# Optimization experiments

Measured on AMD Instinct MI355X. Metric: run time of the kernel, lower is better.

The kernel has to match this reference:

```python
import jax, jax.numpy as jnp
import numpy as np

N = 50000      # num_nodes
DEG = 16       # edges per node
E = N * DEG    # 800k edges
IN_DIM = 512
OUT_DIM = 128


def _glorot(key, shape):
    limit = np.sqrt(6.0 / (shape[0] + shape[1]))
    return jax.random.uniform(key, shape, jnp.float32, -limit, limit)


def setup_inputs() -> dict:
    key = jax.random.key(0)
    k1, k2, k3 = jax.random.split(key, 3)
    x = jax.random.normal(k1, (N, IN_DIM), jnp.float32)
    W = _glorot(k2, (IN_DIM, OUT_DIM))
    a = _glorot(k3, (OUT_DIM, 1))
    # structured, duplicate-free edge list: node i -> (i+1..i+DEG) mod N
    rows = np.repeat(np.arange(N, dtype=np.int32), DEG)
    offs = np.tile(np.arange(1, DEG + 1, dtype=np.int32), N)
    cols = (rows + offs) % N
    edge_index = jnp.asarray(np.stack([rows, cols]), jnp.int32)  # [2, E]
    return {"x": x, "W": W, "a": a, "edge_index": edge_index}


def reference(x, W, a, edge_index):
    # sparse mm (math-identical dense form); dropout_rate=0 -> identity
    h = x @ W                                    # [N, OUT]
    rows, cols = edge_index[0], edge_index[1]
    h_i = h[rows]                                # [E, OUT] gather
    h_j = h[cols]                                # [E, OUT] gather
    scores = jax.nn.relu(jnp.abs(h_i - h_j) @ a)[:, 0]  # [E]
    # sparse row-wise softmax (segment softmax over destination rows)
    m = jax.ops.segment_max(scores, rows, num_segments=N)   # [N]
    p = jnp.exp(scores - m[rows])                            # [E]
    s = jax.ops.segment_sum(p, rows, num_segments=N)         # [N]
    attn = p / s[rows]                                       # [E]
    return h, attn
```

## Files before the change

kernel.cpp:

```cpp
#include <hip/hip_runtime.h>
#include <hip/hip_bf16.h>

#define NNODES 50000
#define DEG 16
#define NEDGES (NNODES * DEG)
#define IND 512
#define OUTD 128

#define BM 64
#define CK 64
#define NCH 8
#define NB 64
#define SROWS 80

typedef __attribute__((ext_vector_type(8))) short bf16x8;
typedef __attribute__((ext_vector_type(4))) float f32x4;

static __device__ __forceinline__ unsigned short f2bf(float f) {
    unsigned u = __builtin_bit_cast(unsigned, f);
    u += 0x7fffu + ((u >> 16) & 1u);
    return (unsigned short)(u >> 16);
}

static __device__ __forceinline__ bf16x8 pack8(float4 a, float4 b) {
    union { unsigned u[4]; bf16x8 v; } r;
    r.u[0] = (unsigned)f2bf(a.x) | ((unsigned)f2bf(a.y) << 16);
    r.u[1] = (unsigned)f2bf(a.z) | ((unsigned)f2bf(a.w) << 16);
    r.u[2] = (unsigned)f2bf(b.x) | ((unsigned)f2bf(b.y) << 16);
    r.u[3] = (unsigned)f2bf(b.z) | ((unsigned)f2bf(b.w) << 16);
    return r.v;
}

__global__ __launch_bounds__(256) void wt_kernel(const float* __restrict__ W,
                                                 unsigned short* __restrict__ Wt) {
    int flat = blockIdx.x * 256 + threadIdx.x;
    int n  = flat >> 7;
    int k4 = flat & 127;
    int k0 = k4 * 4;
    unsigned short v0 = f2bf(W[(k0 + 0) * OUTD + n]);
    unsigned short v1 = f2bf(W[(k0 + 1) * OUTD + n]);
    unsigned short v2 = f2bf(W[(k0 + 2) * OUTD + n]);
    unsigned short v3 = f2bf(W[(k0 + 3) * OUTD + n]);
    uint2 o;
    o.x = (unsigned)v0 | ((unsigned)v1 << 16);
    o.y = (unsigned)v2 | ((unsigned)v3 << 16);
    *reinterpret_cast<uint2*>(&Wt[n * IND + k0]) = o;
}

__global__ __launch_bounds__(256, 2) void gemm_kernel(const float* __restrict__ x,
                                                      const unsigned short* __restrict__ Wt,
                                                      float* __restrict__ h) {
    __shared__ __align__(16) unsigned char lds_[65536];

    const int tid  = threadIdx.x;
    const int lane = tid & 63;
    const int wid  = tid >> 6;
    const int l15  = lane & 15;
    const int kg   = lane >> 4;
    const int base = blockIdx.x * BM;
    const int wr   = wid * 16;

    f32x4 acc[8];
#pragma unroll
    for (int nt = 0; nt < 8; ++nt) acc[nt] = (f32x4){0.f, 0.f, 0.f, 0.f};

    auto stage = [&](int buf, int ch) {
        const int k0 = ch * CK;
#pragma unroll
        for (int p = 0; p < 4; ++p) {
            int f   = p * 256 + tid;
            int row = f >> 4;
            int g   = (f & 15) ^ (row & 7);
            int gr  = base + row; if (gr > NNODES - 1) gr = NNODES - 1;
            const float* gp = &x[(size_t)gr * IND + k0 + g * 4];
            unsigned char* lp = &lds_[(size_t)buf * 16384 + (size_t)f * 16];
            __builtin_amdgcn_global_load_lds((const unsigned int*)gp, (unsigned int*)lp, 16, 0, 0);
        }
#pragma unroll
        for (int p = 0; p < 4; ++p) {
            int f   = p * 256 + tid;
            int col = f >> 3;
            int g   = (f & 7) ^ (col & 7);
            const unsigned short* gp = &Wt[(size_t)col * IND + k0 + g * 8];
            unsigned char* lp = &lds_[32768 + (size_t)buf * 16384 + (size_t)f * 16];
            __builtin_amdgcn_global_load_lds((const unsigned int*)gp, (unsigned int*)lp, 16, 0, 0);
        }
    };

    stage(0, 0);

    int buf = 0;
    for (int ch = 0; ch < NCH; ++ch) {
        if (ch < NCH - 1) {
            stage(buf ^ 1, ch + 1);
            asm volatile("s_waitcnt vmcnt(8)" ::: "memory");
        } else {
            asm volatile("s_waitcnt vmcnt(0)" ::: "memory");
        }
        __builtin_amdgcn_s_barrier();

#pragma unroll
        for (int ks = 0; ks < 2; ++ks) {
            int arow = wr + l15;
            const unsigned char* ab = &lds_[(size_t)buf * 16384 + (size_t)arow * 256];
            int g0 = (ks * 8 + kg * 2) ^ (arow & 7);
            int g1 = (ks * 8 + kg * 2 + 1) ^ (arow & 7);
            float4 a0 = *reinterpret_cast<const float4*>(ab + g0 * 16);
            float4 a1 = *reinterpret_cast<const float4*>(ab + g1 * 16);
            bf16x8 af = pack8(a0, a1);
#pragma unroll
            for (int nt = 0; nt < 8; ++nt) {
                int col = nt * 16 + l15;
                int gB  = (ks * 4 + kg) ^ (col & 7);
                bf16x8 bv = *reinterpret_cast<const bf16x8*>(
                    &lds_[32768 + (size_t)buf * 16384 + (size_t)col * 128 + gB * 16]);
                acc[nt] = __builtin_amdgcn_mfma_f32_16x16x32_bf16(af, bv, acc[nt], 0, 0, 0);
            }
        }
        __builtin_amdgcn_s_barrier();
        buf ^= 1;
    }

#pragma unroll
    for (int q = 0; q < 4; ++q) {
        int grow = base + wr + kg * 4 + q;
        if (grow < NNODES) {
#pragma unroll
            for (int nt = 0; nt < 8; ++nt)
                h[(size_t)grow * OUTD + nt * 16 + l15] = acc[nt][q];
        }
    }
}

__global__ __launch_bounds__(256) void edge_kernel(const float* __restrict__ h,
                                                   const float* __restrict__ a,
                                                   const int* __restrict__ eidx,
                                                   float* __restrict__ attn) {
    extern __shared__ __align__(16) unsigned char hl[];

    const int tid  = threadIdx.x;
    const int base = blockIdx.x * NB;
    const int lane = tid & 63;
    const int wid  = tid >> 6;
    const int j    = lane >> 2;
    const int g    = lane & 3;

    float4 a4[8];
#pragma unroll
    for (int c = 0; c < 8; ++c)
        a4[c] = *reinterpret_cast<const float4*>(&a[c * 16 + g * 4]);

    for (int p = 0; p < 10; ++p) {
        int f    = p * 256 + tid;
        int row  = f >> 5;
        int blkp = f & 31;
        int blk  = blkp ^ ((row & 7) << 2);
        int gr   = base + row;
        if (gr >= NNODES) gr -= NNODES;
        float4 v = *reinterpret_cast<const float4*>(&h[(size_t)gr * OUTD + blk * 4]);
        *reinterpret_cast<float4*>(&hl[f * 16]) = v;
    }
    __syncthreads();

    const int* cols = eidx + NEDGES;
    for (int n = 0; n < 16; ++n) {
        int i = base + wid * 16 + n;
        if (i >= NNODES) break;
        int e   = i * DEG + j;
        int col = cols[e];
        int cr  = col - base;
        if (cr < 0) cr += NNODES;
        int ri = i - base;
        float s = 0.f;
        if (cr < SROWS) {
#pragma unroll
            for (int c = 0; c < 8; ++c) {
                int blk = c * 4 + g;
                float4 hi = *reinterpret_cast<const float4*>(&hl[ri * 512 + ((blk ^ ((ri & 7) << 2)) * 16)]);
                float4 hj = *reinterpret_cast<const float4*>(&hl[cr * 512 + ((blk ^ ((cr & 7) << 2)) * 16)]);
                s = fmaf(fabsf(hi.x - hj.x), a4[c].x, s);
                s = fmaf(fabsf(hi.y - hj.y), a4[c].y, s);
                s = fmaf(fabsf(hi.z - hj.z), a4[c].z, s);
                s = fmaf(fabsf(hi.w - hj.w), a4[c].w, s);
            }
        } else {
#pragma unroll
            for (int c = 0; c < 8; ++c) {
                int blk = c * 4 + g;
                float4 hi = *reinterpret_cast<const float4*>(&hl[ri * 512 + ((blk ^ ((ri & 7) << 2)) * 16)]);
                float4 hj = *reinterpret_cast<const float4*>(&h[(size_t)col * OUTD + blk * 4]);
                s = fmaf(fabsf(hi.x - hj.x), a4[c].x, s);
                s = fmaf(fabsf(hi.y - hj.y), a4[c].y, s);
                s = fmaf(fabsf(hi.z - hj.z), a4[c].z, s);
                s = fmaf(fabsf(hi.w - hj.w), a4[c].w, s);
            }
        }
        s += __shfl_xor(s, 1);
        s += __shfl_xor(s, 2);
        s = fmaxf(s, 0.f);
        float m = s;
        m = fmaxf(m, __shfl_xor(m, 4));
        m = fmaxf(m, __shfl_xor(m, 8));
        m = fmaxf(m, __shfl_xor(m, 16));
        m = fmaxf(m, __shfl_xor(m, 32));
        float pv = __expf(s - m);
        float S = pv;
        S += __shfl_xor(S, 4);
        S += __shfl_xor(S, 8);
        S += __shfl_xor(S, 16);
        S += __shfl_xor(S, 32);
        if (g == 0) attn[e] = pv / S;
    }
}

extern "C" void kernel_launch(void* const* d_in, const int* in_sizes, int n_in,
                              void* d_out, int out_size, void* d_ws, size_t ws_size,
                              hipStream_t stream) {
    const float* x  = (const float*)d_in[0];
    const float* W  = (const float*)d_in[1];
    const float* a  = (const float*)d_in[2];
    const int* eidx = (const int*)d_in[3];
    float* h    = (float*)d_out;
    float* attn = h + (size_t)NNODES * OUTD;
    unsigned short* Wt = (unsigned short*)d_ws;

    hipLaunchKernelGGL(wt_kernel, dim3(64), dim3(256), 0, stream, W, Wt);
    hipLaunchKernelGGL(gemm_kernel, dim3((NNODES + BM - 1) / BM), dim3(256), 0, stream, x, Wt, h);
    hipLaunchKernelGGL(edge_kernel, dim3((NNODES + NB - 1) / NB), dim3(256), SROWS * 512, stream,
                       h, a, eidx, attn);
}
```

Measured before the change: 61.26 us.

## Stage x through registers as bf16 in LDS and split GEMM waves by column

The GEMM now loads x rows into registers one chunk ahead, converts them to bf16 once per block, and writes them to a swizzled LDS buffer, instead of copying fp32 x tiles into LDS and converting per wave. This halves the A-tile LDS footprint, which allows three blocks per CU instead of two. Waves now split the 128 output columns, so each wave does a 64x32 tile with 4x2 MFMAs, rather than each wave taking 16 rows and all columns. The B prefetch is issued after the barrier and one of the two per-chunk barriers is removed. This relies on a single barrier per chunk being enough to stop the next chunk's writes from overwriting buffers still being read, which is a race risk.

```diff
diff --git a/kernel.cpp b/kernel.cpp
--- a/kernel.cpp
+++ b/kernel.cpp
@@ -47,10 +47,10 @@
     *reinterpret_cast<uint2*>(&Wt[n * IND + k0]) = o;
 }
 
-__global__ __launch_bounds__(256, 2) void gemm_kernel(const float* __restrict__ x,
+__global__ __launch_bounds__(256, 3) void gemm_kernel(const float* __restrict__ x,
                                                       const unsigned short* __restrict__ Wt,
                                                       float* __restrict__ h) {
-    __shared__ __align__(16) unsigned char lds_[65536];
+    __shared__ __align__(16) unsigned char lds_[49152];
 
     const int tid  = threadIdx.x;
     const int lane = tid & 63;
@@ -58,76 +58,105 @@
     const int l15  = lane & 15;
     const int kg   = lane >> 4;
     const int base = blockIdx.x * BM;
-    const int wr   = wid * 16;
-
-    f32x4 acc[8];
-#pragma unroll
-    for (int nt = 0; nt < 8; ++nt) acc[nt] = (f32x4){0.f, 0.f, 0.f, 0.f};
-
-    auto stage = [&](int buf, int ch) {
-        const int k0 = ch * CK;
-#pragma unroll
-        for (int p = 0; p < 4; ++p) {
-            int f   = p * 256 + tid;
-            int row = f >> 4;
-            int g   = (f & 15) ^ (row & 7);
-            int gr  = base + row; if (gr > NNODES - 1) gr = NNODES - 1;
-            const float* gp = &x[(size_t)gr * IND + k0 + g * 4];
-            unsigned char* lp = &lds_[(size_t)buf * 16384 + (size_t)f * 16];
-            __builtin_amdgcn_global_load_lds((const unsigned int*)gp, (unsigned int*)lp, 16, 0, 0);
-        }
+    const int wc   = wid * 32;
+
+    const int ar  = tid >> 2;
+    const int ag0 = (tid & 3) * 2;
+    int agr = base + ar; if (agr > NNODES - 1) agr = NNODES - 1;
+    const float* axp = &x[(size_t)agr * IND + ag0 * 8];
+
+    f32x4 acc[4][2];
+#pragma unroll
+    for (int mt = 0; mt < 4; ++mt)
+#pragma unroll
+        for (int nt = 0; nt < 2; ++nt) acc[mt][nt] = (f32x4){0.f, 0.f, 0.f, 0.f};
+
+    float4 rA[2][4];
+
+    auto stageB = [&](int buf, int ch) {
 #pragma unroll
         for (int p = 0; p < 4; ++p) {
             int f   = p * 256 + tid;
             int col = f >> 3;
             int g   = (f & 7) ^ (col & 7);
-            const unsigned short* gp = &Wt[(size_t)col * IND + k0 + g * 8];
-            unsigned char* lp = &lds_[32768 + (size_t)buf * 16384 + (size_t)f * 16];
+            const unsigned short* gp = &Wt[(size_t)col * IND + ch * CK + g * 8];
+            unsigned char* lp = &lds_[16384 + (size_t)buf * 16384 + (size_t)f * 16];
             __builtin_amdgcn_global_load_lds((const unsigned int*)gp, (unsigned int*)lp, 16, 0, 0);
         }
     };
 
-    stage(0, 0);
-
-    int buf = 0;
+    {
+        const float* p = axp;
+        rA[0][0] = *reinterpret_cast<const float4*>(p);
+        rA[0][1] = *reinterpret_cast<const float4*>(p + 4);
+        rA[0][2] = *reinterpret_cast<const float4*>(p + 8);
+        rA[0][3] = *reinterpret_cast<const float4*>(p + 12);
+    }
+    stageB(0, 0);
+
+#pragma unroll
     for (int ch = 0; ch < NCH; ++ch) {
+        const int par = ch & 1;
         if (ch < NCH - 1) {
-            stage(buf ^ 1, ch + 1);
-            asm volatile("s_waitcnt vmcnt(8)" ::: "memory");
+            const float* p = axp + (ch + 1) * CK;
+            rA[par ^ 1][0] = *reinterpret_cast<const float4*>(p);
+            rA[par ^ 1][1] = *reinterpret_cast<const float4*>(p + 4);
+            rA[par ^ 1][2] = *reinterpret_cast<const float4*>(p + 8);
+            rA[par ^ 1][3] = *reinterpret_cast<const float4*>(p + 12);
+            asm volatile("s_waitcnt vmcnt(4)" ::: "memory");
         } else {
             asm volatile("s_waitcnt vmcnt(0)" ::: "memory");
         }
+
+        {
+            bf16x8 q0 = pack8(rA[par][0], rA[par][1]);
+            bf16x8 q1 = pack8(rA[par][2], rA[par][3]);
+            unsigned char* aw = &lds_[(size_t)par * 8192 + (size_t)ar * 128];
+            *reinterpret_cast<bf16x8*>(aw + ((ag0 ^ (ar & 7)) * 16))       = q0;
+            *reinterpret_cast<bf16x8*>(aw + (((ag0 + 1) ^ (ar & 7)) * 16)) = q1;
+        }
+        asm volatile("s_waitcnt lgkmcnt(0)" ::: "memory");
         __builtin_amdgcn_s_barrier();
-
+        asm volatile("" ::: "memory");
+        __builtin_amdgcn_sched_barrier(0);
+
+        if (ch < NCH - 1) stageB(par ^ 1, ch + 1);
+
+        const unsigned char* Ab = &lds_[(size_t)par * 8192];
+        const unsigned char* Bb = &lds_[16384 + (size_t)par * 16384];
 #pragma unroll
         for (int ks = 0; ks < 2; ++ks) {
-            int arow = wr + l15;
-            const unsigned char* ab = &lds_[(size_t)buf * 16384 + (size_t)arow * 256];
-            int g0 = (ks * 8 + kg * 2) ^ (arow & 7);
-            int g1 = (ks * 8 + kg * 2 + 1) ^ (arow & 7);
-            float4 a0 = *reinterpret_cast<const float4*>(ab + g0 * 16);
-            float4 a1 = *reinterpret_cast<const float4*>(ab + g1 * 16);
-            bf16x8 af = pack8(a0, a1);
-#pragma unroll
-            for (int nt = 0; nt < 8; ++nt) {
-                int col = nt * 16 + l15;
-                int gB  = (ks * 4 + kg) ^ (col & 7);
-                bf16x8 bv = *reinterpret_cast<const bf16x8*>(
-                    &lds_[32768 + (size_t)buf * 16384 + (size_t)col * 128 + gB * 16]);
-                acc[nt] = __builtin_amdgcn_mfma_f32_16x16x32_bf16(af, bv, acc[nt], 0, 0, 0);
-            }
-        }
-        __builtin_amdgcn_s_barrier();
-        buf ^= 1;
-    }
-
-#pragma unroll
-    for (int q = 0; q < 4; ++q) {
-        int grow = base + wr + kg * 4 + q;
-        if (grow < NNODES) {
-#pragma unroll
-            for (int nt = 0; nt < 8; ++nt)
-                h[(size_t)grow * OUTD + nt * 16 + l15] = acc[nt][q];
+            bf16x8 af[4], bfv[2];
+#pragma unroll
+            for (int mt = 0; mt < 4; ++mt) {
+                int row = mt * 16 + l15;
+                af[mt] = *reinterpret_cast<const bf16x8*>(
+                    Ab + row * 128 + (((ks * 4 + kg) ^ (row & 7)) * 16));
+            }
+#pragma unroll
+            for (int nt = 0; nt < 2; ++nt) {
+                int col = wc + nt * 16 + l15;
+                bfv[nt] = *reinterpret_cast<const bf16x8*>(
+                    Bb + col * 128 + (((ks * 4 + kg) ^ (col & 7)) * 16));
+            }
+#pragma unroll
+            for (int mt = 0; mt < 4; ++mt)
+#pragma unroll
+                for (int nt = 0; nt < 2; ++nt)
+                    acc[mt][nt] = __builtin_amdgcn_mfma_f32_16x16x32_bf16(af[mt], bfv[nt], acc[mt][nt], 0, 0, 0);
+        }
+    }
+
+#pragma unroll
+    for (int mt = 0; mt < 4; ++mt) {
+#pragma unroll
+        for (int q = 0; q < 4; ++q) {
+            int grow = base + mt * 16 + kg * 4 + q;
+            if (grow < NNODES) {
+#pragma unroll
+                for (int nt = 0; nt < 2; ++nt)
+                    h[(size_t)grow * OUTD + wc + nt * 16 + l15] = acc[mt][nt][q];
+            }
         }
     }
 }
```

After: 62.28 us. Within noise of the previous version (+1.7%).
